# Kernel optimization log

Measured on AMD Instinct MI355X. Metric: run time of the kernel, lower is better.

The kernel has to match this reference:

```python
import jax, jax.numpy as jnp
import numpy as np

B, S, E, H = 2, 2048, 1024, 16
HD = E // H


def setup_inputs() -> dict:
    key = jax.random.key(0)
    ks = jax.random.split(key, 5)
    scale = 1.0 / np.sqrt(E)
    return {
        "query": jax.random.normal(ks[0], (B, S, E), jnp.float32),
        "key": jax.random.normal(ks[1], (B, S, E), jnp.float32),
        "value": jax.random.normal(ks[2], (B, S, E), jnp.float32),
        "qkv_w": jax.random.normal(ks[3], (3 * E, E), jnp.float32) * scale,
        "qkv_b": jnp.zeros((3 * E,), jnp.float32),
        "out_w": jax.random.normal(ks[4], (E, E), jnp.float32) * scale,
        "out_b": jnp.zeros((E,), jnp.float32),
    }


def reference(query, key, value, qkv_w, qkv_b, out_w, out_b):
    # Fused QKV projection from query (module ignores key/value contents)
    qkv = query @ qkv_w.T + qkv_b                      # [B,S,3E]
    qkv = qkv.reshape(B, S, 3, H, HD)
    q = qkv[:, :, 0].transpose(0, 2, 1, 3)             # [B,H,S,HD]
    k = qkv[:, :, 1].transpose(0, 2, 1, 3)
    v = qkv[:, :, 2].transpose(0, 2, 1, 3)
    scaling = 1.0 / np.sqrt(HD)
    scores = jnp.einsum("bhqd,bhkd->bhqk", q, k) * scaling  # [B,H,S,S]
    probs = jax.nn.softmax(scores, axis=-1)
    ctx = jnp.einsum("bhqk,bhkd->bhqd", probs, v)      # [B,H,S,HD]
    ctx = ctx.transpose(0, 2, 1, 3).reshape(B, S, E)
    return ctx @ out_w.T + out_b
```

## Files before the change

### kernel.cpp

```cpp
#include <hip/hip_runtime.h>
#include <hip/hip_bf16.h>
#include <math.h>

#define BB 2
#define SS 2048
#define EE 1024
#define HH 16
#define HD 64
#define NBLK 512

typedef __bf16 bf16;
typedef __bf16 bf16x8 __attribute__((ext_vector_type(8)));
typedef float floatx4 __attribute__((ext_vector_type(4)));
typedef float floatx16 __attribute__((ext_vector_type(16)));

#define MFMA(a, b, c) __builtin_amdgcn_mfma_f32_16x16x32_bf16(a, b, c, 0, 0, 0)
#define MFMA32(a, b, c) __builtin_amdgcn_mfma_f32_32x32x16_bf16(a, b, c, 0, 0, 0)

__device__ inline void async16(const bf16* g, bf16* l) {
    __builtin_amdgcn_global_load_lds(
        (const __attribute__((address_space(1))) void*)g,
        (__attribute__((address_space(3))) void*)l, 16, 0, 0);
}

__device__ inline unsigned cvt_pk_bf16(float a, float b) {
    unsigned r;
    asm("v_cvt_pk_bf16_f32 %0, %1, %2" : "=v"(r) : "v"(a), "v"(b));
    return r;
}

__device__ inline float fast_exp2(float x) {
    float r;
    asm("v_exp_f32 %0, %1" : "=v"(r) : "v"(x));
    return r;
}

__global__ __launch_bounds__(256) void cvt3(
    const float* __restrict__ a, const float* __restrict__ b,
    const float* __restrict__ c,
    bf16* __restrict__ oa, bf16* __restrict__ ob, bf16* __restrict__ oc) {
    const long NA = (long)4096 * 1024, NB = (long)3072 * 1024, NC = (long)1024 * 1024;
    const long total = (NA + NB + NC) >> 2;
    long i = (long)blockIdx.x * blockDim.x + threadIdx.x;
    const long stride = (long)gridDim.x * blockDim.x;
    for (; i < total; i += stride) {
        const long e = i << 2;
        const float* src;
        bf16* dst;
        if (e < NA)           { src = a + e;            dst = oa + e; }
        else if (e < NA + NB) { src = b + (e - NA);     dst = ob + (e - NA); }
        else                  { src = c + (e - NA - NB); dst = oc + (e - NA - NB); }
        float4 v = *(const float4*)src;
        union { bf16 h[4]; uint2 u; } t;
        t.h[0] = (bf16)v.x; t.h[1] = (bf16)v.y; t.h[2] = (bf16)v.z; t.h[3] = (bf16)v.w;
        *(uint2*)dst = t.u;
    }
}

__global__ __launch_bounds__(512, 4) void qkv_gemm(
    const bf16* __restrict__ A, const bf16* __restrict__ W,
    const float* __restrict__ bias,
    bf16* __restrict__ Qw, bf16* __restrict__ Kw, bf16* __restrict__ Vtw) {
    __shared__ __align__(16) bf16 smem[32768];
    const int bid  = blockIdx.x;
    const int tid  = threadIdx.x;
    const int wave = tid >> 6, lane = tid & 63;
    const int quad = lane >> 4, l16 = lane & 15;
    const int wr = wave >> 2, wc = wave & 3;
    const int lr = lane >> 3;
    const int lcs = ((lane & 7) ^ (lr & 7)) * 8;
    const int rsw = (l16 & 7) << 3;
    bf16* As0 = smem;         bf16* As1 = smem + 8192;
    bf16* Bs0 = smem + 16384; bf16* Bs1 = smem + 24576;
    const bool stA = wave < 4;
    const int sw = wave & 3;
    bf16* L0g = (stA ? As0 : Bs0) + sw * 2048 + lane * 8;
    bf16* L1g = (stA ? As1 : Bs1) + sw * 2048 + lane * 8;

    for (int tile = bid; tile < 768; tile += NBLK) {
        const int m0 = (tile / 24) * 128, n0 = (tile % 24) * 128;
        const bf16* G = stA
            ? (A + (long)(m0 + sw * 32 + lr) * 1024 + lcs)
            : (W + (long)(n0 + sw * 32 + lr) * 1024 + lcs);
        floatx4 acc[4][2] = {};
#pragma unroll
        for (int j = 0; j < 4; ++j)
            async16(G + (long)j * 8 * 1024, L0g + j * 512);
        for (int ks = 0; ks < 16; ++ks) {
            __syncthreads();
            if (ks < 15) {
                bf16* Ln = (ks & 1) ? L0g : L1g;
                const int k0 = (ks + 1) * 64;
#pragma unroll
                for (int j = 0; j < 4; ++j)
                    async16(G + (long)j * 8 * 1024 + k0, Ln + j * 512);
            }
            const bf16* Ac = (ks & 1) ? As1 : As0;
            const bf16* Bc = (ks & 1) ? Bs1 : Bs0;
#pragma unroll
            for (int c = 0; c < 2; ++c) {
                bf16x8 af[4], bfr[2];
#pragma unroll
                for (int mi = 0; mi < 4; ++mi)
                    af[mi] = *(const bf16x8*)&Ac[(wr * 64 + mi * 16 + l16) * 64 + ((c * 32 + quad * 8) ^ rsw)];
#pragma unroll
                for (int ni = 0; ni < 2; ++ni)
                    bfr[ni] = *(const bf16x8*)&Bc[(wc * 32 + ni * 16 + l16) * 64 + ((c * 32 + quad * 8) ^ rsw)];
#pragma unroll
                for (int mi = 0; mi < 4; ++mi)
#pragma unroll
                    for (int ni = 0; ni < 2; ++ni)
                        acc[mi][ni] = MFMA(af[mi], bfr[ni], acc[mi][ni]);
            }
        }
#pragma unroll
        for (int mi = 0; mi < 4; ++mi)
#pragma unroll
            for (int ni = 0; ni < 2; ++ni) {
                const int n = n0 + wc * 32 + ni * 16 + l16;
                const float bn = bias[n];
                const int sel = n >> 10;
                const int e = n & 1023, h = e >> 6, d = e & 63;
                if (sel == 2) {
                    const int m_base = m0 + wr * 64 + mi * 16 + quad * 4;
                    const int b = m_base >> 11, s0 = m_base & 2047;
                    union { bf16 h4[4]; uint2 u; } t;
#pragma unroll
                    for (int r = 0; r < 4; ++r)
                        t.h4[r] = (bf16)(acc[mi][ni][r] + bn);
                    *(uint2*)&Vtw[((long)(b * HH + h) * HD + d) * SS + s0] = t.u;
                } else {
#pragma unroll
                    for (int r = 0; r < 4; ++r) {
                        const int m = m0 + wr * 64 + mi * 16 + quad * 4 + r;
                        const int b = m >> 11, s = m & 2047;
                        const float v = acc[mi][ni][r] + bn;
                        if (sel == 0)
                            Qw[((long)(b * HH + h) * SS + s) * HD + d] = (bf16)(v * 0.18033688f);
                        else
                            Kw[((long)(b * HH + h) * SS + s) * HD + d] = (bf16)v;
                    }
                }
            }
        __syncthreads();
    }
}

__global__ __launch_bounds__(512) void attn(
    const bf16* __restrict__ Qw, const bf16* __restrict__ Kw,
    const bf16* __restrict__ Vtw, bf16* __restrict__ ctxw) {
    extern __shared__ __align__(16) bf16 smem[];

    const int tid = threadIdx.x;
    const int wave = tid >> 6, lane = tid & 63;
    const int grp = wave >> 2, w4 = wave & 3;
    const int l5 = lane & 31, hi = lane >> 5;

    const int d_  = blockIdx.y * gridDim.x + blockIdx.x;
    const int j_  = d_ >> 3;
    const int bh  = (d_ & 7) * 4 + (j_ >> 4);
    const int qb  = j_ & 15;

    const bf16* Qh = Qw  + (long)bh * SS * HD;
    const bf16* Kh = Kw  + (long)bh * SS * HD;
    const bf16* Vh = Vtw + (long)bh * HD * SS;

    const int qbase = qb * 128 + w4 * 32;
    bf16x8 qf[4];
#pragma unroll
    for (int d0 = 0; d0 < 4; ++d0)
        qf[d0] = *(const bf16x8*)&Qh[(long)(qbase + l5) * HD + d0 * 16 + hi * 8];

    floatx16 ctx0 = {}, ctx1 = {};
    float lsum = 0.f;

    const int wrow = w4 * 8 + (lane >> 3);
    const int sch  = ((lane & 7) ^ ((lane >> 3) & 7)) * 8;
    const int kvo  = grp * 1024;
    const bf16* Kg0 = Kh + (long)(kvo + wrow) * HD + sch;
    const bf16* Kg1 = Kh + (long)(kvo + 32 + wrow) * HD + sch;
    const bf16* Vg0 = Vh + (long)wrow * SS + kvo + sch;
    const bf16* Vg1 = Vh + (long)(32 + wrow) * SS + kvo + sch;
    const int ldst = w4 * 512 + lane * 8;
    const int rswz = (l5 & 7) << 3;

    bf16* Kt0 = smem + (grp * 2 + 0) * 4096;
    bf16* Kt1 = smem + (grp * 2 + 1) * 4096;
    bf16* Vt0 = smem + 16384 + (grp * 2 + 0) * 4096;
    bf16* Vt1 = smem + 16384 + (grp * 2 + 1) * 4096;

    async16(Kg0, Kt0 + ldst);
    async16(Kg1, Kt0 + ldst + 2048);
    async16(Vg0, Vt0 + ldst);
    async16(Vg1, Vt0 + ldst + 2048);

    for (int kt = 0; kt < 16; ++kt) {
        __syncthreads();
        if (kt < 15) {
            bf16* Kn = (kt & 1) ? Kt0 : Kt1;
            bf16* Vn = (kt & 1) ? Vt0 : Vt1;
            const long ko = (long)(kt + 1) * 64;
            async16(Kg0 + ko * HD, Kn + ldst);
            async16(Kg1 + ko * HD, Kn + ldst + 2048);
            async16(Vg0 + ko,      Vn + ldst);
            async16(Vg1 + ko,      Vn + ldst + 2048);
        }
        const bf16* Kc = (kt & 1) ? Kt1 : Kt0;
        const bf16* Vc = (kt & 1) ? Vt1 : Vt0;

        floatx16 sf[2];
#pragma unroll
        for (int kb = 0; kb < 2; ++kb) {
            floatx16 s = {};
            __builtin_amdgcn_s_setprio(1);
#pragma unroll
            for (int d0 = 0; d0 < 4; ++d0) {
                const bf16x8 af = *(const bf16x8*)
                    &Kc[(kb * 32 + l5) * 64 + ((d0 * 16 + hi * 8) ^ rswz)];
                s = MFMA32(af, qf[d0], s);
            }
            __builtin_amdgcn_s_setprio(0);
            sf[kb] = s;
        }

#pragma unroll
        for (int kb = 0; kb < 2; ++kb) {
#pragma unroll
            for (int r = 0; r < 16; ++r) {
                const float p = fast_exp2(sf[kb][r]);
                sf[kb][r] = p;
                lsum += p;
            }
            unsigned w[8];
#pragma unroll
            for (int i = 0; i < 8; ++i)
                w[i] = cvt_pk_bf16(sf[kb][2 * i], sf[kb][2 * i + 1]);
            asm("v_permlane32_swap_b32 %0, %1" : "+v"(w[0]), "+v"(w[2]));
            asm("v_permlane32_swap_b32 %0, %1" : "+v"(w[1]), "+v"(w[3]));
            asm("v_permlane32_swap_b32 %0, %1" : "+v"(w[4]), "+v"(w[6]));
            asm("v_permlane32_swap_b32 %0, %1" : "+v"(w[5]), "+v"(w[7]));
            union { unsigned u[4]; bf16x8 v; } pa0 = {{w[0], w[1], w[2], w[3]}},
                                               pa1 = {{w[4], w[5], w[6], w[7]}};
#pragma unroll
            for (int kc = 0; kc < 2; ++kc) {
                const bf16x8 pa = kc ? pa1.v : pa0.v;
                const int kcol = kb * 32 + kc * 16 + hi * 8;
                const bf16x8 vf0 = *(const bf16x8*)&Vc[l5 * 64 + (kcol ^ rswz)];
                const bf16x8 vf1 = *(const bf16x8*)&Vc[(32 + l5) * 64 + (kcol ^ rswz)];
                __builtin_amdgcn_s_setprio(1);
                ctx0 = MFMA32(pa, vf0, ctx0);
                ctx1 = MFMA32(pa, vf1, ctx1);
                __builtin_amdgcn_s_setprio(0);
            }
        }
    }

    __syncthreads();
    float* cb = (float*)smem;
    float* lb = (float*)(smem + 16384);
    if (grp == 1) {
#pragma unroll
        for (int r = 0; r < 16; ++r) {
            cb[(w4 * 32 + r) * 64 + lane]      = ctx0[r];
            cb[(w4 * 32 + 16 + r) * 64 + lane] = ctx1[r];
        }
        lb[w4 * 64 + lane] = lsum;
    }
    __syncthreads();
    if (grp == 0) {
        lsum += lb[w4 * 64 + lane];
#pragma unroll
        for (int r = 0; r < 16; ++r) {
            ctx0[r] += cb[(w4 * 32 + r) * 64 + lane];
            ctx1[r] += cb[(w4 * 32 + 16 + r) * 64 + lane];
        }
        const float rs  = lsum + __shfl_xor(lsum, 32, 64);
        const float inv = 1.0f / rs;

        const int b = bh >> 4, h = bh & 15;
#pragma unroll
        for (int r = 0; r < 16; ++r) {
            const int qrow = (r & 3) + 8 * (r >> 2) + 4 * hi;
            const float iq = __shfl(inv, qrow, 64);
            const long base = ((long)b * SS + qbase + qrow) * EE + h * HD;
            ctxw[base + l5]      = (bf16)(ctx0[r] * iq);
            ctxw[base + 32 + l5] = (bf16)(ctx1[r] * iq);
        }
    }
}

__global__ __launch_bounds__(512, 4) void out_gemm(
    const bf16* __restrict__ A, const bf16* __restrict__ W,
    const float* __restrict__ bias, float* __restrict__ out) {
    __shared__ __align__(16) bf16 smem[24576];
    const int tid  = threadIdx.x;
    const int wave = tid >> 6, lane = tid & 63;
    const int quad = lane >> 4, l16 = lane & 15;
    const int wr = wave >> 2, wc = wave & 3;
    const int m0 = blockIdx.y * 64, n0 = blockIdx.x * 128;
    const int lr = lane >> 3;
    const int lcs = ((lane & 7) ^ (lr & 7)) * 8;
    const int rsw = (l16 & 7) << 3;
    bf16* As0 = smem;         bf16* As1 = smem + 4096;
    bf16* Bs0 = smem + 8192;  bf16* Bs1 = smem + 16384;

    const bool stA = wave < 2;
    const bool doStage = (wave < 2) || (wave >= 4);
    const int swA = wave & 1, swB = wave & 3;
    const bf16* G = stA
        ? (A + (long)(m0 + swA * 32 + lr) * 1024 + lcs)
        : (W + (long)(n0 + swB * 32 + lr) * 1024 + lcs);
    bf16* L0 = stA ? As0 + swA * 2048 + lane * 8 : Bs0 + swB * 2048 + lane * 8;
    bf16* L1 = stA ? As1 + swA * 2048 + lane * 8 : Bs1 + swB * 2048 + lane * 8;

    floatx4 acc[2][2] = {};

    if (doStage)
#pragma unroll
        for (int j = 0; j < 4; ++j)
            async16(G + (long)j * 8 * 1024, L0 + j * 512);

    for (int ks = 0; ks < 16; ++ks) {
        __syncthreads();
        if (ks < 15 && doStage) {
            bf16* Ln = (ks & 1) ? L0 : L1;
            const int k0 = (ks + 1) * 64;
#pragma unroll
            for (int j = 0; j < 4; ++j)
                async16(G + (long)j * 8 * 1024 + k0, Ln + j * 512);
        }
        const bf16* Ac = (ks & 1) ? As1 : As0;
        const bf16* Bc = (ks & 1) ? Bs1 : Bs0;
#pragma unroll
        for (int c = 0; c < 2; ++c) {
            bf16x8 af[2], bfr[2];
#pragma unroll
            for (int mi = 0; mi < 2; ++mi)
                af[mi] = *(const bf16x8*)&Ac[(wr * 32 + mi * 16 + l16) * 64 + ((c * 32 + quad * 8) ^ rsw)];
#pragma unroll
            for (int ni = 0; ni < 2; ++ni)
                bfr[ni] = *(const bf16x8*)&Bc[(wc * 32 + ni * 16 + l16) * 64 + ((c * 32 + quad * 8) ^ rsw)];
#pragma unroll
            for (int mi = 0; mi < 2; ++mi)
#pragma unroll
                for (int ni = 0; ni < 2; ++ni)
                    acc[mi][ni] = MFMA(af[mi], bfr[ni], acc[mi][ni]);
        }
    }

#pragma unroll
    for (int mi = 0; mi < 2; ++mi)
#pragma unroll
        for (int ni = 0; ni < 2; ++ni) {
            const int n = n0 + wc * 32 + ni * 16 + l16;
            const float bn = bias[n];
#pragma unroll
            for (int r = 0; r < 4; ++r) {
                const int m = m0 + wr * 32 + mi * 16 + quad * 4 + r;
                out[(long)m * 1024 + n] = acc[mi][ni][r] + bn;
            }
        }
}

extern "C" void kernel_launch(void* const* d_in, const int* in_sizes, int n_in,
                              void* d_out, int out_size, void* d_ws, size_t ws_size,
                              hipStream_t stream) {
    const float* query = (const float*)d_in[0];
    const float* qkv_w = (const float*)d_in[3];
    const float* qkv_b = (const float*)d_in[4];
    const float* out_w = (const float*)d_in[5];
    const float* out_b = (const float*)d_in[6];

    const long NTOK = (long)BB * SS;
    bf16* qb   = (bf16*)d_ws;
    bf16* wqb  = qb  + NTOK * EE;
    bf16* owb  = wqb + (long)3 * EE * EE;
    bf16* Qw   = owb + (long)EE * EE;
    bf16* Kw   = Qw  + NTOK * EE;
    bf16* Vtw  = Kw  + NTOK * EE;
    bf16* ctxw = qb;
    float* out = (float*)d_out;

    cvt3<<<2048, 256, 0, stream>>>(query, qkv_w, out_w, qb, wqb, owb);
    qkv_gemm<<<dim3(NBLK), dim3(512), 0, stream>>>(qb, wqb, qkv_b, Qw, Kw, Vtw);
    attn<<<dim3(16, 32), 512, 65536, stream>>>(Qw, Kw, Vtw, ctxw);
    out_gemm<<<dim3(8, 64), 512, 0, stream>>>(ctxw, owb, out_b, out);
}
```

Measured before the change: 189.0 us.

## Software-pipeline attention PV MFMAs one tile behind QK with triple-buffered V

```diff
diff --git a/kernel.cpp b/kernel.cpp
--- a/kernel.cpp
+++ b/kernel.cpp
@@ -149,7 +149,7 @@
 __global__ __launch_bounds__(512) void attn(
     const bf16* __restrict__ Qw, const bf16* __restrict__ Kw,
     const bf16* __restrict__ Vtw, bf16* __restrict__ ctxw) {
-    extern __shared__ __align__(16) bf16 smem[];
+    __shared__ __align__(16) bf16 smem[40960];
 
     const int tid = threadIdx.x;
     const int wave = tid >> 6, lane = tid & 63;
@@ -186,19 +186,26 @@
 
     bf16* Kt0 = smem + (grp * 2 + 0) * 4096;
     bf16* Kt1 = smem + (grp * 2 + 1) * 4096;
-    bf16* Vt0 = smem + 16384 + (grp * 2 + 0) * 4096;
-    bf16* Vt1 = smem + 16384 + (grp * 2 + 1) * 4096;
+    bf16* Vt0 = smem + 16384 + (grp * 3 + 0) * 4096;
+    bf16* Vt1 = smem + 16384 + (grp * 3 + 1) * 4096;
+    bf16* Vt2 = smem + 16384 + (grp * 3 + 2) * 4096;
 
     async16(Kg0, Kt0 + ldst);
     async16(Kg1, Kt0 + ldst + 2048);
     async16(Vg0, Vt0 + ldst);
     async16(Vg1, Vt0 + ldst + 2048);
 
+    bf16x8 paP[4];
+    int vcur = 0;
+
     for (int kt = 0; kt < 16; ++kt) {
+        const int vnext = (vcur == 2) ? 0 : vcur + 1;
+        const int vprev = (vcur == 0) ? 2 : vcur - 1;
         __syncthreads();
+
         if (kt < 15) {
             bf16* Kn = (kt & 1) ? Kt0 : Kt1;
-            bf16* Vn = (kt & 1) ? Vt0 : Vt1;
+            bf16* Vn = (vnext == 0) ? Vt0 : ((vnext == 1) ? Vt1 : Vt2);
             const long ko = (long)(kt + 1) * 64;
             async16(Kg0 + ko * HD, Kn + ldst);
             async16(Kg1 + ko * HD, Kn + ldst + 2048);
@@ -206,7 +213,6 @@
             async16(Vg1 + ko,      Vn + ldst + 2048);
         }
         const bf16* Kc = (kt & 1) ? Kt1 : Kt0;
-        const bf16* Vc = (kt & 1) ? Vt1 : Vt0;
 
         floatx16 sf[2];
 #pragma unroll
@@ -221,6 +227,20 @@
             }
             __builtin_amdgcn_s_setprio(0);
             sf[kb] = s;
+        }
+
+        if (kt > 0) {
+            const bf16* Vp = (vprev == 0) ? Vt0 : ((vprev == 1) ? Vt1 : Vt2);
+            __builtin_amdgcn_s_setprio(1);
+#pragma unroll
+            for (int i = 0; i < 4; ++i) {
+                const int kcol = (i >> 1) * 32 + (i & 1) * 16 + hi * 8;
+                const bf16x8 vf0 = *(const bf16x8*)&Vp[l5 * 64 + (kcol ^ rswz)];
+                const bf16x8 vf1 = *(const bf16x8*)&Vp[(32 + l5) * 64 + (kcol ^ rswz)];
+                ctx0 = MFMA32(paP[i], vf0, ctx0);
+                ctx1 = MFMA32(paP[i], vf1, ctx1);
+            }
+            __builtin_amdgcn_s_setprio(0);
         }
 
 #pragma unroll
@@ -241,18 +261,26 @@
             asm("v_permlane32_swap_b32 %0, %1" : "+v"(w[5]), "+v"(w[7]));
             union { unsigned u[4]; bf16x8 v; } pa0 = {{w[0], w[1], w[2], w[3]}},
                                                pa1 = {{w[4], w[5], w[6], w[7]}};
-#pragma unroll
-            for (int kc = 0; kc < 2; ++kc) {
-                const bf16x8 pa = kc ? pa1.v : pa0.v;
-                const int kcol = kb * 32 + kc * 16 + hi * 8;
-                const bf16x8 vf0 = *(const bf16x8*)&Vc[l5 * 64 + (kcol ^ rswz)];
-                const bf16x8 vf1 = *(const bf16x8*)&Vc[(32 + l5) * 64 + (kcol ^ rswz)];
-                __builtin_amdgcn_s_setprio(1);
-                ctx0 = MFMA32(pa, vf0, ctx0);
-                ctx1 = MFMA32(pa, vf1, ctx1);
-                __builtin_amdgcn_s_setprio(0);
-            }
-        }
+            paP[kb * 2 + 0] = pa0.v;
+            paP[kb * 2 + 1] = pa1.v;
+        }
+
+        vcur = vnext;
+    }
+
+    {
+        const int vprev = (vcur == 0) ? 2 : vcur - 1;
+        const bf16* Vp = (vprev == 0) ? Vt0 : ((vprev == 1) ? Vt1 : Vt2);
+        __builtin_amdgcn_s_setprio(1);
+#pragma unroll
+        for (int i = 0; i < 4; ++i) {
+            const int kcol = (i >> 1) * 32 + (i & 1) * 16 + hi * 8;
+            const bf16x8 vf0 = *(const bf16x8*)&Vp[l5 * 64 + (kcol ^ rswz)];
+            const bf16x8 vf1 = *(const bf16x8*)&Vp[(32 + l5) * 64 + (kcol ^ rswz)];
+            ctx0 = MFMA32(paP[i], vf0, ctx0);
+            ctx1 = MFMA32(paP[i], vf1, ctx1);
+        }
+        __builtin_amdgcn_s_setprio(0);
     }
 
     __syncthreads();
@@ -383,6 +411,6 @@
 
     cvt3<<<2048, 256, 0, stream>>>(query, qkv_w, out_w, qb, wqb, owb);
     qkv_gemm<<<dim3(NBLK), dim3(512), 0, stream>>>(qb, wqb, qkv_b, Qw, Kw, Vtw);
-    attn<<<dim3(16, 32), 512, 65536, stream>>>(Qw, Kw, Vtw, ctxw);
+    attn<<<dim3(16, 32), 512, 0, stream>>>(Qw, Kw, Vtw, ctxw);
     out_gemm<<<dim3(8, 64), 512, 0, stream>>>(ctxw, owb, out_b, out);
 }
```

New measurement: 202.8 us. +7.3%, slower.

## Split attention KV range across four wave groups with single-buffered tiles

Applied to the files above, without the earlier changes.

```diff
diff --git a/kernel.cpp b/kernel.cpp
--- a/kernel.cpp
+++ b/kernel.cpp
@@ -146,10 +146,10 @@
     }
 }
 
-__global__ __launch_bounds__(512) void attn(
+__global__ __launch_bounds__(1024, 8) void attn(
     const bf16* __restrict__ Qw, const bf16* __restrict__ Kw,
     const bf16* __restrict__ Vtw, bf16* __restrict__ ctxw) {
-    extern __shared__ __align__(16) bf16 smem[];
+    __shared__ __align__(16) bf16 smem[34816];
 
     const int tid = threadIdx.x;
     const int wave = tid >> 6, lane = tid & 63;
@@ -176,7 +176,7 @@
 
     const int wrow = w4 * 8 + (lane >> 3);
     const int sch  = ((lane & 7) ^ ((lane >> 3) & 7)) * 8;
-    const int kvo  = grp * 1024;
+    const int kvo  = grp * 512;
     const bf16* Kg0 = Kh + (long)(kvo + wrow) * HD + sch;
     const bf16* Kg1 = Kh + (long)(kvo + 32 + wrow) * HD + sch;
     const bf16* Vg0 = Vh + (long)wrow * SS + kvo + sch;
@@ -184,29 +184,16 @@
     const int ldst = w4 * 512 + lane * 8;
     const int rswz = (l5 & 7) << 3;
 
-    bf16* Kt0 = smem + (grp * 2 + 0) * 4096;
-    bf16* Kt1 = smem + (grp * 2 + 1) * 4096;
-    bf16* Vt0 = smem + 16384 + (grp * 2 + 0) * 4096;
-    bf16* Vt1 = smem + 16384 + (grp * 2 + 1) * 4096;
-
-    async16(Kg0, Kt0 + ldst);
-    async16(Kg1, Kt0 + ldst + 2048);
-    async16(Vg0, Vt0 + ldst);
-    async16(Vg1, Vt0 + ldst + 2048);
-
-    for (int kt = 0; kt < 16; ++kt) {
+    bf16* Kt = smem + grp * 4096;
+    bf16* Vt = smem + 16384 + grp * 4096;
+
+    async16(Kg0, Kt + ldst);
+    async16(Kg1, Kt + ldst + 2048);
+    async16(Vg0, Vt + ldst);
+    async16(Vg1, Vt + ldst + 2048);
+
+    for (int kt = 0; kt < 8; ++kt) {
         __syncthreads();
-        if (kt < 15) {
-            bf16* Kn = (kt & 1) ? Kt0 : Kt1;
-            bf16* Vn = (kt & 1) ? Vt0 : Vt1;
-            const long ko = (long)(kt + 1) * 64;
-            async16(Kg0 + ko * HD, Kn + ldst);
-            async16(Kg1 + ko * HD, Kn + ldst + 2048);
-            async16(Vg0 + ko,      Vn + ldst);
-            async16(Vg1 + ko,      Vn + ldst + 2048);
-        }
-        const bf16* Kc = (kt & 1) ? Kt1 : Kt0;
-        const bf16* Vc = (kt & 1) ? Vt1 : Vt0;
 
         floatx16 sf[2];
 #pragma unroll
@@ -216,7 +203,7 @@
 #pragma unroll
             for (int d0 = 0; d0 < 4; ++d0) {
                 const bf16x8 af = *(const bf16x8*)
-                    &Kc[(kb * 32 + l5) * 64 + ((d0 * 16 + hi * 8) ^ rswz)];
+                    &Kt[(kb * 32 + l5) * 64 + ((d0 * 16 + hi * 8) ^ rswz)];
                 s = MFMA32(af, qf[d0], s);
             }
             __builtin_amdgcn_s_setprio(0);
@@ -245,35 +232,76 @@
             for (int kc = 0; kc < 2; ++kc) {
                 const bf16x8 pa = kc ? pa1.v : pa0.v;
                 const int kcol = kb * 32 + kc * 16 + hi * 8;
-                const bf16x8 vf0 = *(const bf16x8*)&Vc[l5 * 64 + (kcol ^ rswz)];
-                const bf16x8 vf1 = *(const bf16x8*)&Vc[(32 + l5) * 64 + (kcol ^ rswz)];
+                const bf16x8 vf0 = *(const bf16x8*)&Vt[l5 * 64 + (kcol ^ rswz)];
+                const bf16x8 vf1 = *(const bf16x8*)&Vt[(32 + l5) * 64 + (kcol ^ rswz)];
                 __builtin_amdgcn_s_setprio(1);
                 ctx0 = MFMA32(pa, vf0, ctx0);
                 ctx1 = MFMA32(pa, vf1, ctx1);
                 __builtin_amdgcn_s_setprio(0);
             }
         }
-    }
-
-    __syncthreads();
-    float* cb = (float*)smem;
-    float* lb = (float*)(smem + 16384);
+
+        __syncthreads();
+        if (kt < 7) {
+            const long ko = (long)(kt + 1) * 64;
+            async16(Kg0 + ko * HD, Kt + ldst);
+            async16(Kg1 + ko * HD, Kt + ldst + 2048);
+            async16(Vg0 + ko,      Vt + ldst);
+            async16(Vg1 + ko,      Vt + ldst + 2048);
+        }
+    }
+
+    float* cb0 = (float*)smem;
+    float* cb1 = (float*)(smem + 16384);
+    float* lsb = (float*)(smem + 32768);
+    lsb[(grp * 4 + w4) * 64 + lane] = lsum;
     if (grp == 1) {
 #pragma unroll
         for (int r = 0; r < 16; ++r) {
-            cb[(w4 * 32 + r) * 64 + lane]      = ctx0[r];
-            cb[(w4 * 32 + 16 + r) * 64 + lane] = ctx1[r];
-        }
-        lb[w4 * 64 + lane] = lsum;
+            cb0[(w4 * 32 + r) * 64 + lane]      = ctx0[r];
+            cb0[(w4 * 32 + 16 + r) * 64 + lane] = ctx1[r];
+        }
+    }
+    if (grp == 3) {
+#pragma unroll
+        for (int r = 0; r < 16; ++r) {
+            cb1[(w4 * 32 + r) * 64 + lane]      = ctx0[r];
+            cb1[(w4 * 32 + 16 + r) * 64 + lane] = ctx1[r];
+        }
     }
     __syncthreads();
     if (grp == 0) {
-        lsum += lb[w4 * 64 + lane];
-#pragma unroll
-        for (int r = 0; r < 16; ++r) {
-            ctx0[r] += cb[(w4 * 32 + r) * 64 + lane];
-            ctx1[r] += cb[(w4 * 32 + 16 + r) * 64 + lane];
-        }
+#pragma unroll
+        for (int r = 0; r < 16; ++r) {
+            ctx0[r] += cb0[(w4 * 32 + r) * 64 + lane];
+            ctx1[r] += cb0[(w4 * 32 + 16 + r) * 64 + lane];
+        }
+    }
+    if (grp == 2) {
+#pragma unroll
+        for (int r = 0; r < 16; ++r) {
+            ctx0[r] += cb1[(w4 * 32 + r) * 64 + lane];
+            ctx1[r] += cb1[(w4 * 32 + 16 + r) * 64 + lane];
+        }
+    }
+    __syncthreads();
+    if (grp == 2) {
+#pragma unroll
+        for (int r = 0; r < 16; ++r) {
+            cb0[(w4 * 32 + r) * 64 + lane]      = ctx0[r];
+            cb0[(w4 * 32 + 16 + r) * 64 + lane] = ctx1[r];
+        }
+    }
+    __syncthreads();
+    if (grp == 0) {
+#pragma unroll
+        for (int r = 0; r < 16; ++r) {
+            ctx0[r] += cb0[(w4 * 32 + r) * 64 + lane];
+            ctx1[r] += cb0[(w4 * 32 + 16 + r) * 64 + lane];
+        }
+        lsum += lsb[(1 * 4 + w4) * 64 + lane]
+              + lsb[(2 * 4 + w4) * 64 + lane]
+              + lsb[(3 * 4 + w4) * 64 + lane];
         const float rs  = lsum + __shfl_xor(lsum, 32, 64);
         const float inv = 1.0f / rs;
 
@@ -383,6 +411,6 @@
 
     cvt3<<<2048, 256, 0, stream>>>(query, qkv_w, out_w, qb, wqb, owb);
     qkv_gemm<<<dim3(NBLK), dim3(512), 0, stream>>>(qb, wqb, qkv_b, Qw, Kw, Vtw);
-    attn<<<dim3(16, 32), 512, 65536, stream>>>(Qw, Kw, Vtw, ctxw);
+    attn<<<dim3(16, 32), 1024, 0, stream>>>(Qw, Kw, Vtw, ctxw);
     out_gemm<<<dim3(8, 64), 512, 0, stream>>>(ctxw, owb, out_b, out);
 }
```

New measurement: 477.3 us. 152% more time.
